# Kernel optimization log

Measured on AMD Instinct MI355X. Metric: run time of the kernel, lower is better.

Reference implementation:

```python
import jax, jax.numpy as jnp
import numpy as np

NEG_INF = -9e15  # matches torch zero_vec constant
ALPHA = 0.2      # leaky relu slope


def setup_inputs() -> dict:
    key = jax.random.key(0)
    k1, k2, k3, k4, k5 = jax.random.split(key, 5)
    B, N, F_in, F_out = 8, 2048, 128, 64
    h = jax.random.normal(k1, (B, N, F_in), dtype=jnp.float32)
    adj = jax.random.randint(k2, (B, N, N), 0, 2, dtype=jnp.int32)
    # learned params: W (no bias), a = Linear(2*F_out, 1) split into a1, a2
    W = jax.random.normal(k3, (F_in, F_out), dtype=jnp.float32) / np.sqrt(F_in)
    a1 = jax.random.normal(k4, (F_out,), dtype=jnp.float32) / np.sqrt(2 * F_out)
    a2 = jax.random.normal(k5, (F_out,), dtype=jnp.float32) / np.sqrt(2 * F_out)
    return {"h": h, "adj": adj, "W": W, "a1": a1, "a2": a2}


def reference(h, adj, W, a1, a2):
    # Wh: (B, N, F_out)
    Wh = jnp.einsum('bnf,fo->bno', h, W)
    # a([Wh_i || Wh_j]) == a1·Wh_i + a2·Wh_j  (Linear has no bias)
    s1 = Wh @ a1  # (B, N) contribution of source node i
    s2 = Wh @ a2  # (B, N) contribution of target node j
    e = jax.nn.leaky_relu(s1[:, :, None] + s2[:, None, :], negative_slope=ALPHA)  # (B,N,N)
    scores = jnp.where(adj > 0, e, NEG_INF)
    attn = jax.nn.softmax(scores, axis=2)  # dropout inactive (eval mode)
    h_prime = jnp.einsum('bij,bjo->bio', attn, Wh)
    return jax.nn.elu(h_prime)
```

## Files before the change

### kernel.cpp

```cpp
#include <hip/hip_runtime.h>
#include <hip/hip_bf16.h>
#include <cmath>

#define NB 8
#define NN 2048
#define FIN 128
#define FOUT 64
#define GAT_ALPHA 0.2f

typedef __attribute__((ext_vector_type(8))) short short8;
typedef __attribute__((ext_vector_type(4))) float f32x4;

static __device__ __forceinline__ ushort f2bf(float x) {
    __hip_bfloat16 hb = __float2bfloat16(x);
    return __builtin_bit_cast(ushort, hb);
}
static __device__ __forceinline__ short8 pack8(const float4 a, const float4 b) {
    short8 r;
    r[0] = (short)f2bf(a.x); r[1] = (short)f2bf(a.y); r[2] = (short)f2bf(a.z); r[3] = (short)f2bf(a.w);
    r[4] = (short)f2bf(b.x); r[5] = (short)f2bf(b.y); r[6] = (short)f2bf(b.z); r[7] = (short)f2bf(b.w);
    return r;
}

__global__ void wt_kernel(const float* __restrict__ W, const float* __restrict__ a1,
                          const float* __restrict__ a2, ushort* __restrict__ WT,
                          float* __restrict__ wa) {
    const int t = threadIdx.x;
    const int o = t & 63, kg = t >> 6;
#pragma unroll
    for (int kk = 0; kk < 32; ++kk) {
        const int k = kg * 32 + kk;
        WT[o * FIN + k] = f2bf(W[k * FOUT + o]);
    }
    if (t < FIN) {
        float x1 = 0.f, x2 = 0.f;
        for (int o2 = 0; o2 < FOUT; ++o2) {
            const float w = W[t * FOUT + o2];
            x1 = fmaf(w, a1[o2], x1);
            x2 = fmaf(w, a2[o2], x2);
        }
        wa[t] = x1; wa[FIN + t] = x2;
    }
}

__global__ __launch_bounds__(256) void wh_kernel(const float* __restrict__ h,
                                                 const ushort* __restrict__ WT,
                                                 const float* __restrict__ wa,
                                                 ushort* __restrict__ whT,
                                                 float* __restrict__ s1,
                                                 float* __restrict__ s2) {
    const int t = threadIdx.x, w = t >> 6, lane = t & 63;
    const int rrow = lane & 15, kg = lane >> 4;
    const int j0 = blockIdx.x * 16;
    const int b = j0 >> 11, jloc = j0 & (NN - 1);
    const float* hrow = h + (size_t)(j0 + rrow) * FIN + kg * 8;

    float4 hv[8];
    short8 af[4];
#pragma unroll
    for (int ks = 0; ks < 4; ++ks) {
        hv[2 * ks]     = *(const float4*)(hrow + ks * 32);
        hv[2 * ks + 1] = *(const float4*)(hrow + ks * 32 + 4);
        af[ks] = pack8(hv[2 * ks], hv[2 * ks + 1]);
    }
    f32x4 acc = {0.f, 0.f, 0.f, 0.f};
#pragma unroll
    for (int ks = 0; ks < 4; ++ks) {
        const short8 bf = *(const short8*)(WT + (size_t)(w * 16 + rrow) * FIN + ks * 32 + kg * 8);
        acc = __builtin_amdgcn_mfma_f32_16x16x32_bf16(af[ks], bf, acc, 0, 0, 0);
    }
#pragma unroll
    for (int q = 0; q < 4; ++q)
        whT[(((size_t)b * FOUT + w * 16 + rrow) << 11) + jloc + kg * 4 + q] = f2bf(acc[q]);

    if (w == 0) {
        float p1 = 0.f, p2 = 0.f;
#pragma unroll
        for (int ks = 0; ks < 4; ++ks) {
#pragma unroll
            for (int e = 0; e < 8; ++e) {
                const float4 hq = hv[2 * ks + (e >> 2)];
                const float x = (e & 3) == 0 ? hq.x : (e & 3) == 1 ? hq.y : (e & 3) == 2 ? hq.z : hq.w;
                const int k = ks * 32 + kg * 8 + e;
                p1 = fmaf(x, wa[k], p1);
                p2 = fmaf(x, wa[FIN + k], p2);
            }
        }
        p1 += __shfl_xor(p1, 16); p1 += __shfl_xor(p1, 32);
        p2 += __shfl_xor(p2, 16); p2 += __shfl_xor(p2, 32);
        if (lane < 16) { s1[j0 + lane] = p1; s2[j0 + lane] = p2; }
    }
}

__global__ __launch_bounds__(256) void attn_kernel(const int* __restrict__ adj,
                                                   const ushort* __restrict__ whT,
                                                   const float* __restrict__ s1,
                                                   const float* __restrict__ s2,
                                                   float* __restrict__ pnum,
                                                   float* __restrict__ pden) {
    __shared__ float smem[4 * 16 * FOUT];
    __shared__ float den[4][16];
    const int t = threadIdx.x, w = t >> 6, lane = t & 63;
    const int rrow = lane & 15, kg = lane >> 4;
    const int b = blockIdx.x >> 8, blk = blockIdx.x & 255;
    const int i0 = (blk >> 1) << 4, half = blk & 1;
    const int jh = half * (NN / 2);

    for (int idx = t; idx < NN / 2; idx += 256) smem[idx] = s2[b * NN + jh + idx];
    const float s1v = s1[b * NN + i0 + rrow];
    const int* adjRow = adj + ((size_t)(b * NN + i0 + rrow)) * NN + jh;
    const ushort* whB = whT + (size_t)b * FOUT * NN + jh;
    __syncthreads();

    f32x4 acc[4] = {{0,0,0,0},{0,0,0,0},{0,0,0,0},{0,0,0,0}};
    float dsum = 0.f;
    const int jb0 = w * 256 + kg * 8;

    int4 buf[2][2];
    buf[0][0] = *(const int4*)(adjRow + jb0);
    buf[0][1] = *(const int4*)(adjRow + jb0 + 4);
    buf[1][0] = *(const int4*)(adjRow + jb0 + 32);
    buf[1][1] = *(const int4*)(adjRow + jb0 + 36);

#pragma unroll
    for (int step = 0; step < 8; ++step) {
        const int jb = jb0 + step * 32;
        const int4 c0 = buf[step & 1][0];
        const int4 c1 = buf[step & 1][1];
        if (step + 2 < 8) {
            buf[step & 1][0] = *(const int4*)(adjRow + jb + 64);
            buf[step & 1][1] = *(const int4*)(adjRow + jb + 68);
        }
        const float4 sv0 = *(const float4*)(smem + jb);
        const float4 sv1 = *(const float4*)(smem + jb + 4);
        const int   a[8] = {c0.x, c0.y, c0.z, c0.w, c1.x, c1.y, c1.z, c1.w};
        const float s[8] = {sv0.x, sv0.y, sv0.z, sv0.w, sv1.x, sv1.y, sv1.z, sv1.w};
        short8 af;
        float ds = 0.f;
#pragma unroll
        for (int r = 0; r < 8; ++r) {
            const float x = s1v + s[r];
            const float e = __expf(fmaxf(x, GAT_ALPHA * x));
            const float p = (a[r] > 0) ? e : 0.f;
            ds += p;
            af[r] = (short)f2bf(p);
        }
        dsum += ds;
#pragma unroll
        for (int nt = 0; nt < 4; ++nt) {
            const short8 bf = *(const short8*)(whB + ((size_t)(nt * 16 + rrow) << 11) + jb);
            acc[nt] = __builtin_amdgcn_mfma_f32_16x16x32_bf16(af, bf, acc[nt], 0, 0, 0);
        }
    }
    dsum += __shfl_xor(dsum, 16);
    dsum += __shfl_xor(dsum, 32);
    if (lane < 16) den[w][lane] = dsum;
    __syncthreads();

#pragma unroll
    for (int nt = 0; nt < 4; ++nt)
#pragma unroll
        for (int q = 0; q < 4; ++q)
            smem[(w * 16 + kg * 4 + q) * FOUT + nt * 16 + rrow] = acc[nt][q];
    __syncthreads();

    const size_t obase = (((size_t)half * NB + b) * NN + i0) * FOUT;
#pragma unroll
    for (int rep = 0; rep < 4; ++rep) {
        const int idx = rep * 256 + t;
        const int r = idx >> 6, o = idx & 63;
        pnum[obase + (size_t)r * FOUT + o] = smem[r * FOUT + o] + smem[(16 + r) * FOUT + o]
                                          + smem[(32 + r) * FOUT + o] + smem[(48 + r) * FOUT + o];
    }
    if (t < 16) pden[((size_t)half * NB + b) * NN + i0 + t] =
        den[0][t] + den[1][t] + den[2][t] + den[3][t];
}

__global__ __launch_bounds__(256) void reduce_kernel(const float* __restrict__ pnum,
                                                     const float* __restrict__ pden,
                                                     float* __restrict__ out) {
    const int idx = blockIdx.x * 256 + threadIdx.x;
    const int bi = idx >> 6;
    const float num = pnum[idx] + pnum[idx + (size_t)NB * NN * FOUT];
    const float d = pden[bi] + pden[bi + NB * NN];
    const float v = num / d;
    out[idx] = v > 0.f ? v : expm1f(v);
}

extern "C" void kernel_launch(void* const* d_in, const int* in_sizes, int n_in,
                              void* d_out, int out_size, void* d_ws, size_t ws_size,
                              hipStream_t stream) {
    const float* h   = (const float*)d_in[0];
    const int*   adj = (const int*)d_in[1];
    const float* W   = (const float*)d_in[2];
    const float* a1  = (const float*)d_in[3];
    const float* a2  = (const float*)d_in[4];
    float* out = (float*)d_out;

    char* ws = (char*)d_ws;
    ushort* whT = (ushort*)ws;  ws += (size_t)NB * FOUT * NN * sizeof(ushort);
    ushort* WT  = (ushort*)ws;  ws += (size_t)FOUT * FIN * sizeof(ushort);
    float*  wa  = (float*)ws;   ws += (size_t)2 * FIN * sizeof(float);
    float*  s1  = (float*)ws;   ws += (size_t)NB * NN * sizeof(float);
    float*  s2  = (float*)ws;   ws += (size_t)NB * NN * sizeof(float);
    float*  pnum = (float*)ws;  ws += (size_t)2 * NB * NN * FOUT * sizeof(float);
    float*  pden = (float*)ws;  ws += (size_t)2 * NB * NN * sizeof(float);

    wt_kernel<<<1, 256, 0, stream>>>(W, a1, a2, WT, wa);
    wh_kernel<<<NB * NN / 16, 256, 0, stream>>>(h, WT, wa, whT, s1, s2);
    attn_kernel<<<NB * 256, 256, 0, stream>>>(adj, whT, s1, s2, pnum, pden);
    reduce_kernel<<<NB * NN * FOUT / 256, 256, 0, stream>>>(pnum, pden, out);
}
```

Baseline: 237.1 us.

## Prefetch s2 and Wh fragments in registers, compute denominator via MFMA

The attention kernel now reads s2 straight from global memory into a double-buffered register pipeline and prefetches the Wh B-fragments one step ahead, alongside the adjacency loads. This removes the LDS staging pass for s2 and its barrier. The softmax denominator is now accumulated by an extra MFMA against a ones vector, which uses the bf16-rounded probabilities, instead of scalar adds and shuffles. Smaller tweaks spread the W·a precompute over all threads and split the s1/s2 dot products across two waves in wh_kernel. In exchange the kernel holds more registers, which may lower occupancy.

```diff
diff --git a/kernel.cpp b/kernel.cpp
--- a/kernel.cpp
+++ b/kernel.cpp
@@ -32,15 +32,18 @@
         const int k = kg * 32 + kk;
         WT[o * FIN + k] = f2bf(W[k * FOUT + o]);
     }
-    if (t < FIN) {
-        float x1 = 0.f, x2 = 0.f;
-        for (int o2 = 0; o2 < FOUT; ++o2) {
-            const float w = W[t * FOUT + o2];
-            x1 = fmaf(w, a1[o2], x1);
-            x2 = fmaf(w, a2[o2], x2);
-        }
-        wa[t] = x1; wa[FIN + t] = x2;
-    }
+    const int k = t >> 1, hf = t & 1;
+    float x1 = 0.f, x2 = 0.f;
+#pragma unroll
+    for (int oo = 0; oo < 32; ++oo) {
+        const int o2 = hf * 32 + oo;
+        const float w = W[k * FOUT + o2];
+        x1 = fmaf(w, a1[o2], x1);
+        x2 = fmaf(w, a2[o2], x2);
+    }
+    x1 += __shfl_xor(x1, 1);
+    x2 += __shfl_xor(x2, 1);
+    if (hf == 0) { wa[k] = x1; wa[FIN + k] = x2; }
 }
 
 __global__ __launch_bounds__(256) void wh_kernel(const float* __restrict__ h,
@@ -73,22 +76,22 @@
     for (int q = 0; q < 4; ++q)
         whT[(((size_t)b * FOUT + w * 16 + rrow) << 11) + jloc + kg * 4 + q] = f2bf(acc[q]);
 
-    if (w == 0) {
-        float p1 = 0.f, p2 = 0.f;
+    if (w == 1 || w == 2) {
+        const float* wap = wa + (w == 2 ? FIN : 0);
+        float p = 0.f;
 #pragma unroll
         for (int ks = 0; ks < 4; ++ks) {
 #pragma unroll
             for (int e = 0; e < 8; ++e) {
                 const float4 hq = hv[2 * ks + (e >> 2)];
                 const float x = (e & 3) == 0 ? hq.x : (e & 3) == 1 ? hq.y : (e & 3) == 2 ? hq.z : hq.w;
-                const int k = ks * 32 + kg * 8 + e;
-                p1 = fmaf(x, wa[k], p1);
-                p2 = fmaf(x, wa[FIN + k], p2);
+                p = fmaf(x, wap[ks * 32 + kg * 8 + e], p);
             }
         }
-        p1 += __shfl_xor(p1, 16); p1 += __shfl_xor(p1, 32);
-        p2 += __shfl_xor(p2, 16); p2 += __shfl_xor(p2, 32);
-        if (lane < 16) { s1[j0 + lane] = p1; s2[j0 + lane] = p2; }
+        p += __shfl_xor(p, 16); p += __shfl_xor(p, 32);
+        if (lane < 16) {
+            if (w == 1) s1[j0 + lane] = p; else s2[j0 + lane] = p;
+        }
     }
 }
 
@@ -98,70 +101,77 @@
                                                    const float* __restrict__ s2,
                                                    float* __restrict__ pnum,
                                                    float* __restrict__ pden) {
-    __shared__ float smem[4 * 16 * FOUT];
-    __shared__ float den[4][16];
+    __shared__ float red[4 * 16 * FOUT];
+    __shared__ float denl[4][16];
     const int t = threadIdx.x, w = t >> 6, lane = t & 63;
     const int rrow = lane & 15, kg = lane >> 4;
     const int b = blockIdx.x >> 8, blk = blockIdx.x & 255;
     const int i0 = (blk >> 1) << 4, half = blk & 1;
     const int jh = half * (NN / 2);
 
-    for (int idx = t; idx < NN / 2; idx += 256) smem[idx] = s2[b * NN + jh + idx];
     const float s1v = s1[b * NN + i0 + rrow];
+    const float* s2g = s2 + b * NN + jh;
     const int* adjRow = adj + ((size_t)(b * NN + i0 + rrow)) * NN + jh;
     const ushort* whB = whT + (size_t)b * FOUT * NN + jh;
-    __syncthreads();
+    const int jb0 = w * 256 + kg * 8;
+
+    short8 ones;
+#pragma unroll
+    for (int r = 0; r < 8; ++r) ones[r] = (short)0x3F80;
 
     f32x4 acc[4] = {{0,0,0,0},{0,0,0,0},{0,0,0,0},{0,0,0,0}};
-    float dsum = 0.f;
-    const int jb0 = w * 256 + kg * 8;
-
-    int4 buf[2][2];
-    buf[0][0] = *(const int4*)(adjRow + jb0);
-    buf[0][1] = *(const int4*)(adjRow + jb0 + 4);
-    buf[1][0] = *(const int4*)(adjRow + jb0 + 32);
-    buf[1][1] = *(const int4*)(adjRow + jb0 + 36);
+    f32x4 accd = {0,0,0,0};
+
+    int4   ab[2][2];
+    float4 sb[2][2];
+    short8 wb[2][4];
+    ab[0][0] = *(const int4*)(adjRow + jb0);
+    ab[0][1] = *(const int4*)(adjRow + jb0 + 4);
+    sb[0][0] = *(const float4*)(s2g + jb0);
+    sb[0][1] = *(const float4*)(s2g + jb0 + 4);
+#pragma unroll
+    for (int nt = 0; nt < 4; ++nt)
+        wb[0][nt] = *(const short8*)(whB + ((nt * 16 + rrow) << 11) + jb0);
 
 #pragma unroll
     for (int step = 0; step < 8; ++step) {
-        const int jb = jb0 + step * 32;
-        const int4 c0 = buf[step & 1][0];
-        const int4 c1 = buf[step & 1][1];
-        if (step + 2 < 8) {
-            buf[step & 1][0] = *(const int4*)(adjRow + jb + 64);
-            buf[step & 1][1] = *(const int4*)(adjRow + jb + 68);
-        }
-        const float4 sv0 = *(const float4*)(smem + jb);
-        const float4 sv1 = *(const float4*)(smem + jb + 4);
-        const int   a[8] = {c0.x, c0.y, c0.z, c0.w, c1.x, c1.y, c1.z, c1.w};
-        const float s[8] = {sv0.x, sv0.y, sv0.z, sv0.w, sv1.x, sv1.y, sv1.z, sv1.w};
+        const int cur = step & 1, nxt = cur ^ 1;
+        if (step < 7) {
+            const int jb = jb0 + (step + 1) * 32;
+            ab[nxt][0] = *(const int4*)(adjRow + jb);
+            ab[nxt][1] = *(const int4*)(adjRow + jb + 4);
+            sb[nxt][0] = *(const float4*)(s2g + jb);
+            sb[nxt][1] = *(const float4*)(s2g + jb + 4);
+#pragma unroll
+            for (int nt = 0; nt < 4; ++nt)
+                wb[nxt][nt] = *(const short8*)(whB + ((nt * 16 + rrow) << 11) + jb);
+        }
+        const int   aa[8] = {ab[cur][0].x, ab[cur][0].y, ab[cur][0].z, ab[cur][0].w,
+                             ab[cur][1].x, ab[cur][1].y, ab[cur][1].z, ab[cur][1].w};
+        const float ss[8] = {sb[cur][0].x, sb[cur][0].y, sb[cur][0].z, sb[cur][0].w,
+                             sb[cur][1].x, sb[cur][1].y, sb[cur][1].z, sb[cur][1].w};
         short8 af;
-        float ds = 0.f;
 #pragma unroll
         for (int r = 0; r < 8; ++r) {
-            const float x = s1v + s[r];
+            const float x = s1v + ss[r];
             const float e = __expf(fmaxf(x, GAT_ALPHA * x));
-            const float p = (a[r] > 0) ? e : 0.f;
-            ds += p;
-            af[r] = (short)f2bf(p);
-        }
-        dsum += ds;
-#pragma unroll
-        for (int nt = 0; nt < 4; ++nt) {
-            const short8 bf = *(const short8*)(whB + ((size_t)(nt * 16 + rrow) << 11) + jb);
-            acc[nt] = __builtin_amdgcn_mfma_f32_16x16x32_bf16(af, bf, acc[nt], 0, 0, 0);
-        }
-    }
-    dsum += __shfl_xor(dsum, 16);
-    dsum += __shfl_xor(dsum, 32);
-    if (lane < 16) den[w][lane] = dsum;
-    __syncthreads();
+            af[r] = (short)f2bf(aa[r] > 0 ? e : 0.f);
+        }
+#pragma unroll
+        for (int nt = 0; nt < 4; ++nt)
+            acc[nt] = __builtin_amdgcn_mfma_f32_16x16x32_bf16(af, wb[cur][nt], acc[nt], 0, 0, 0);
+        accd = __builtin_amdgcn_mfma_f32_16x16x32_bf16(af, ones, accd, 0, 0, 0);
+    }
 
 #pragma unroll
     for (int nt = 0; nt < 4; ++nt)
 #pragma unroll
         for (int q = 0; q < 4; ++q)
-            smem[(w * 16 + kg * 4 + q) * FOUT + nt * 16 + rrow] = acc[nt][q];
+            red[(w * 16 + kg * 4 + q) * FOUT + nt * 16 + rrow] = acc[nt][q];
+    if (rrow == 0) {
+#pragma unroll
+        for (int q = 0; q < 4; ++q) denl[w][kg * 4 + q] = accd[q];
+    }
     __syncthreads();
 
     const size_t obase = (((size_t)half * NB + b) * NN + i0) * FOUT;
@@ -169,11 +179,11 @@
     for (int rep = 0; rep < 4; ++rep) {
         const int idx = rep * 256 + t;
         const int r = idx >> 6, o = idx & 63;
-        pnum[obase + (size_t)r * FOUT + o] = smem[r * FOUT + o] + smem[(16 + r) * FOUT + o]
-                                          + smem[(32 + r) * FOUT + o] + smem[(48 + r) * FOUT + o];
+        pnum[obase + (size_t)r * FOUT + o] = red[r * FOUT + o] + red[(16 + r) * FOUT + o]
+                                          + red[(32 + r) * FOUT + o] + red[(48 + r) * FOUT + o];
     }
     if (t < 16) pden[((size_t)half * NB + b) * NN + i0 + t] =
-        den[0][t] + den[1][t] + den[2][t] + den[3][t];
+        denl[0][t] + denl[1][t] + denl[2][t] + denl[3][t];
 }
 
 __global__ __launch_bounds__(256) void reduce_kernel(const float* __restrict__ pnum,
```

Result: no change. 239.7 us (+1.1%).
